# Kernel tuning notes

Hardware: AMD Instinct MI355X
Metric: run time of the kernel (lower is better)

Reference implementation:

```python
import jax, jax.numpy as jnp
import numpy as np

B, N, C, H = 4, 2048, 1024, 16
D = C // H

def setup_inputs() -> dict:
    key = jax.random.key(0)
    k1, k2, k3 = jax.random.split(key, 3)
    x = jax.random.normal(k1, (B, N, C), dtype=jnp.float32)
    w_qkv = jax.random.normal(k2, (C, 3 * C), dtype=jnp.float32) * (C ** -0.5)
    w_proj = jax.random.normal(k3, (C, C), dtype=jnp.float32) * (C ** -0.5)
    b_proj = jnp.zeros((C,), dtype=jnp.float32)
    return {"x": x, "w_qkv": w_qkv, "w_proj": w_proj, "b_proj": b_proj}

def reference(x, w_qkv, w_proj, b_proj):
    scale = D ** -0.5
    qkv = x @ w_qkv                                   # [B,N,3C]
    qkv = qkv.reshape(B, N, 3, H, D).transpose(2, 0, 3, 1, 4)  # [3,B,H,N,D]
    q, k, v = qkv[0], qkv[1], qkv[2]
    attn = jnp.einsum('bhnd,bhmd->bhnm', q, k) * scale  # [B,H,N,N]
    attn = jax.nn.softmax(attn, axis=-1)
    o = jnp.einsum('bhnm,bhmd->bhnd', attn, v)          # [B,H,N,D]
    o = o.transpose(0, 2, 1, 3).reshape(B, N, C)
    return o @ w_proj + b_proj
```

## Files before the change

### kernel.cpp

```cpp
#include <hip/hip_runtime.h>
#include <hip/hip_bf16.h>


#define B_ 4
#define N_ 2048
#define C_ 1024
#define H_ 16
#define D_ 64
#define KVB 128
#define MCONST 24.0f

typedef __attribute__((ext_vector_type(8))) __bf16 bf16x8;
typedef __attribute__((ext_vector_type(4))) float f32x4;
typedef unsigned int u32;

__device__ inline unsigned short f2bf(float f) {
  __bf16 h = (__bf16)f;
  return __builtin_bit_cast(unsigned short, h);
}

__device__ __forceinline__ void gld16(const void* g, void* l) {
  __builtin_amdgcn_global_load_lds(
      (const __attribute__((address_space(1))) u32*)g,
      (__attribute__((address_space(3))) u32*)l, 16, 0, 0);
}

__global__ __launch_bounds__(256) void cvt_bf16_kernel(
    const float* __restrict__ in, unsigned short* __restrict__ out) {
  int i = (blockIdx.x * 256 + threadIdx.x) * 8;
  float4 f0 = *(const float4*)&in[i];
  float4 f1 = *(const float4*)&in[i + 4];
  ushort4 h0, h1;
  h0.x = f2bf(f0.x); h0.y = f2bf(f0.y); h0.z = f2bf(f0.z); h0.w = f2bf(f0.w);
  h1.x = f2bf(f1.x); h1.y = f2bf(f1.y); h1.z = f2bf(f1.z); h1.w = f2bf(f1.w);
  *(ushort4*)&out[i] = h0;
  *(ushort4*)&out[i + 4] = h1;
}

__global__ __launch_bounds__(256) void transpose_cvt_kernel(
    const float* __restrict__ in, unsigned short* __restrict__ out,
    int K, int Nn) {
  __shared__ float tile[32][33];
  const int t = threadIdx.x;
  const int k0 = blockIdx.y * 32, n0 = blockIdx.x * 32;
  {
    int r = t >> 3, c = (t & 7) * 4;
    float4 f = *(const float4*)&in[(size_t)(k0 + r) * Nn + n0 + c];
    tile[r][c + 0] = f.x; tile[r][c + 1] = f.y;
    tile[r][c + 2] = f.z; tile[r][c + 3] = f.w;
  }
  __syncthreads();
  {
    int nr = t >> 3, kc = (t & 7) * 4;
    ushort4 h;
    h.x = f2bf(tile[kc + 0][nr]);
    h.y = f2bf(tile[kc + 1][nr]);
    h.z = f2bf(tile[kc + 2][nr]);
    h.w = f2bf(tile[kc + 3][nr]);
    *(ushort4*)&out[(size_t)(n0 + nr) * K + k0 + kc] = h;
  }
}

__global__ __launch_bounds__(256) void transpose_v_kernel(
    const unsigned short* __restrict__ vb, unsigned short* __restrict__ vtb) {
  __shared__ u32 tile[64][65];
  const int tid = threadIdx.x;
  const int n0 = blockIdx.x * 64;
  const int bh = blockIdx.y;
  const size_t base = (size_t)bh * N_ * D_;
#pragma unroll
  for (int i = 0; i < 2; i++) {
    int id = i * 256 + tid;
    int row = id >> 3, c8 = id & 7;
    uint4 v = *(const uint4*)&vb[base + (size_t)(n0 + row) * D_ + c8 * 8];
    const unsigned short* pv = (const unsigned short*)&v;
#pragma unroll
    for (int j = 0; j < 8; j++) tile[row][c8 * 8 + j] = pv[j];
  }
  __syncthreads();
#pragma unroll
  for (int i = 0; i < 2; i++) {
    int id = i * 256 + tid;
    int d = id >> 3, nc = id & 7;
    uint4 o;
    unsigned short* po = (unsigned short*)&o;
#pragma unroll
    for (int j = 0; j < 8; j++) po[j] = (unsigned short)tile[nc * 8 + j][d];
    *(uint4*)&vtb[base + (size_t)d * N_ + n0 + nc * 8] = o;
  }
}

template<int MODE>
__global__ __launch_bounds__(256) void gemm128_kernel(
    const unsigned short* __restrict__ A, const unsigned short* __restrict__ Bt,
    const float* __restrict__ bias,
    unsigned short* __restrict__ qb, unsigned short* __restrict__ kb,
    unsigned short* __restrict__ vb, float* __restrict__ outp,
    int M, int K, int Nout)
{
  __shared__ unsigned short Al[128 * 64];
  __shared__ unsigned short Bl[128 * 64];
  const int tid = threadIdx.x;
  const int w = tid >> 6, lane = tid & 63;
  const int l15 = lane & 15, lk = lane >> 4;
  const int wr = w >> 1, wc = w & 1;
  const int n0 = blockIdx.x * 128, m0 = blockIdx.y * 128;
  const int srow = tid >> 3;
  const int scol = (tid & 7) * 8;

  f32x4 acc[4][4];
#pragma unroll
  for (int m = 0; m < 4; m++)
#pragma unroll
    for (int n = 0; n < 4; n++) acc[m][n] = f32x4{0.f, 0.f, 0.f, 0.f};

  for (int kt = 0; kt < K; kt += 64) {
#pragma unroll
    for (int i = 0; i < 4; i++)
      gld16(&A[(size_t)(m0 + i * 32 + srow) * K + kt + scol],
            &Al[i * 2048 + w * 512]);
#pragma unroll
    for (int i = 0; i < 4; i++)
      gld16(&Bt[(size_t)(n0 + i * 32 + srow) * K + kt + scol],
            &Bl[i * 2048 + w * 512]);
    __syncthreads();

#pragma unroll
    for (int kk = 0; kk < 2; kk++) {
      bf16x8 af[4], bf[4];
#pragma unroll
      for (int m = 0; m < 4; m++)
        af[m] = *(const bf16x8*)&Al[(wr * 64 + m * 16 + l15) * 64 + kk * 32 + lk * 8];
#pragma unroll
      for (int n = 0; n < 4; n++)
        bf[n] = *(const bf16x8*)&Bl[(wc * 64 + n * 16 + l15) * 64 + kk * 32 + lk * 8];
#pragma unroll
      for (int m = 0; m < 4; m++)
#pragma unroll
        for (int n = 0; n < 4; n++)
          acc[m][n] = __builtin_amdgcn_mfma_f32_16x16x32_bf16(af[m], bf[n], acc[m][n], 0, 0, 0);
    }
    __syncthreads();
  }

  if (MODE == 0) {
#pragma unroll
    for (int n = 0; n < 4; n++) {
      int c = n0 + wc * 64 + n * 16 + l15;
      int tsel = c >> 10, h = (c >> 6) & 15, d = c & 63;
      unsigned short* dst = (tsel == 0) ? qb : (tsel == 1 ? kb : vb);
      float sc = (tsel == 0) ? 0.125f * 1.44269504088896340736f : 1.0f;
#pragma unroll
      for (int m = 0; m < 4; m++) {
#pragma unroll
        for (int r = 0; r < 4; r++) {
          int row = m0 + wr * 64 + m * 16 + lk * 4 + r;
          int b = row >> 11, nn = row & 2047;
          dst[(((size_t)(b * 16 + h)) * 2048 + nn) * 64 + d] = f2bf(acc[m][n][r] * sc);
        }
      }
    }
  } else {
#pragma unroll
    for (int n = 0; n < 4; n++) {
      int c = n0 + wc * 64 + n * 16 + l15;
      float bv = bias[c];
#pragma unroll
      for (int m = 0; m < 4; m++) {
#pragma unroll
        for (int r = 0; r < 4; r++) {
          int row = m0 + wr * 64 + m * 16 + lk * 4 + r;
          outp[(size_t)row * Nout + c] = acc[m][n][r] + bv;
        }
      }
    }
  }
}

__global__ __launch_bounds__(256) void flash_kernel(
    const unsigned short* __restrict__ qb, const unsigned short* __restrict__ kb,
    const unsigned short* __restrict__ vtb, unsigned short* __restrict__ ob)
{
  __shared__ unsigned short Kl[KVB * 64];
  __shared__ unsigned short Vl[64 * KVB];
  __shared__ unsigned short Pl[64][136];
  const int tid = threadIdx.x;
  const int w = tid >> 6;
  const int lane = tid & 63;
  const int l15 = lane & 15, lk = lane >> 4;
  const int q0 = blockIdx.x * 64;
  const int bh = blockIdx.y;
  const size_t base = (size_t)bh * N_ * D_;
  const unsigned short* Qg = qb + base;
  const unsigned short* Kg = kb + base;
  const unsigned short* Vtg = vtb + base;

  const int k_r  = tid >> 3;
  const int k_sl = (tid & 7) ^ (k_r & 7);
  const int v_r  = tid >> 4;
  const int v_sl = ((tid & 15) & 8) | ((tid & 7) ^ (v_r & 7));

  bf16x8 qf[2];
#pragma unroll
  for (int kk = 0; kk < 2; kk++)
    qf[kk] = *(const bf16x8*)&Qg[(size_t)(q0 + w * 16 + l15) * 64 + kk * 32 + lk * 8];

  f32x4 acc_o[4];
#pragma unroll
  for (int i = 0; i < 4; i++) acc_o[i] = f32x4{0.f, 0.f, 0.f, 0.f};
  float lrow[4];
#pragma unroll
  for (int r = 0; r < 4; r++) lrow[r] = 0.f;

  const int swz = (l15 & 7) << 3;
  const int prswz = (l15 & 8) << 1;

  for (int kv0 = 0; kv0 < N_; kv0 += KVB) {
#pragma unroll
    for (int i = 0; i < 4; i++)
      gld16(&Kg[(size_t)(kv0 + i * 32 + k_r) * 64 + k_sl * 8],
            &Kl[i * 2048 + w * 512]);
#pragma unroll
    for (int i = 0; i < 4; i++)
      gld16(&Vtg[(size_t)(i * 16 + v_r) * N_ + kv0 + v_sl * 8],
            &Vl[i * 2048 + w * 512]);
    __syncthreads();

    f32x4 sa[8];
#pragma unroll
    for (int i = 0; i < 8; i++)
      sa[i] = f32x4{-MCONST, -MCONST, -MCONST, -MCONST};
    __builtin_amdgcn_s_setprio(1);
#pragma unroll
    for (int kk = 0; kk < 2; kk++) {
#pragma unroll
      for (int nf = 0; nf < 8; nf++) {
        bf16x8 b = *(const bf16x8*)&Kl[(nf * 16 + l15) * 64 + ((kk * 32 + lk * 8) ^ swz)];
        sa[nf] = __builtin_amdgcn_mfma_f32_16x16x32_bf16(qf[kk], b, sa[nf], 0, 0, 0);
      }
    }
    __builtin_amdgcn_s_setprio(0);

#pragma unroll
    for (int r = 0; r < 4; r++) {
      float p0 = __builtin_amdgcn_exp2f(sa[0][r]);
      float p1 = __builtin_amdgcn_exp2f(sa[1][r]);
      float p2 = __builtin_amdgcn_exp2f(sa[2][r]);
      float p3 = __builtin_amdgcn_exp2f(sa[3][r]);
      float p4 = __builtin_amdgcn_exp2f(sa[4][r]);
      float p5 = __builtin_amdgcn_exp2f(sa[5][r]);
      float p6 = __builtin_amdgcn_exp2f(sa[6][r]);
      float p7 = __builtin_amdgcn_exp2f(sa[7][r]);
      lrow[r] += ((p0 + p1) + (p2 + p3)) + ((p4 + p5) + (p6 + p7));
      int prow = w * 16 + lk * 4 + r;
      int pswz = (prow & 8) << 1;
      Pl[prow][(0   + l15) ^ pswz] = f2bf(p0);
      Pl[prow][(16  + l15) ^ pswz] = f2bf(p1);
      Pl[prow][(32  + l15) ^ pswz] = f2bf(p2);
      Pl[prow][(48  + l15) ^ pswz] = f2bf(p3);
      Pl[prow][(64  + l15) ^ pswz] = f2bf(p4);
      Pl[prow][(80  + l15) ^ pswz] = f2bf(p5);
      Pl[prow][(96  + l15) ^ pswz] = f2bf(p6);
      Pl[prow][(112 + l15) ^ pswz] = f2bf(p7);
    }

    __builtin_amdgcn_s_setprio(1);
#pragma unroll
    for (int kk = 0; kk < 4; kk++) {
      bf16x8 a = *(const bf16x8*)&Pl[w * 16 + l15][(kk * 32 + lk * 8) ^ prswz];
#pragma unroll
      for (int nf = 0; nf < 4; nf++) {
        bf16x8 b = *(const bf16x8*)&Vl[(nf * 16 + l15) * 128 + ((kk * 32 + lk * 8) ^ swz)];
        acc_o[nf] = __builtin_amdgcn_mfma_f32_16x16x32_bf16(a, b, acc_o[nf], 0, 0, 0);
      }
    }
    __builtin_amdgcn_s_setprio(0);
    __syncthreads();
  }

#pragma unroll
  for (int r = 0; r < 4; r++) {
    float rs = lrow[r];
    rs += __shfl_xor(rs, 1);
    rs += __shfl_xor(rs, 2);
    rs += __shfl_xor(rs, 4);
    rs += __shfl_xor(rs, 8);
    lrow[r] = rs;
  }

  const int b = bh >> 4, h = bh & 15;
#pragma unroll
  for (int r = 0; r < 4; r++) {
    float inv = 1.0f / lrow[r];
    int n = q0 + w * 16 + lk * 4 + r;
    size_t obase = (((size_t)b * N_ + n) * H_ + h) * D_;
#pragma unroll
    for (int nf = 0; nf < 4; nf++)
      ob[obase + nf * 16 + l15] = f2bf(acc_o[nf][r] * inv);
  }
}

extern "C" void kernel_launch(void* const* d_in, const int* in_sizes, int n_in,
                              void* d_out, int out_size, void* d_ws, size_t ws_size,
                              hipStream_t stream) {
  const float* x      = (const float*)d_in[0];
  const float* w_qkv  = (const float*)d_in[1];
  const float* w_proj = (const float*)d_in[2];
  const float* b_proj = (const float*)d_in[3];
  float* out = (float*)d_out;

  const size_t qsz = (size_t)B_ * H_ * N_ * D_;
  unsigned short* qb     = (unsigned short*)d_ws;
  unsigned short* kb     = qb + qsz;
  unsigned short* vb     = kb + qsz;
  unsigned short* vtb    = vb + qsz;
  unsigned short* xbf    = vtb + qsz;
  unsigned short* ob     = xbf;
  unsigned short* wqkv_t = xbf + qsz;
  unsigned short* wproj_t= wqkv_t + (size_t)3072 * 1024;

  cvt_bf16_kernel<<<4096, 256, 0, stream>>>(x, xbf);
  transpose_cvt_kernel<<<dim3(3072 / 32, 1024 / 32), 256, 0, stream>>>(w_qkv, wqkv_t, 1024, 3072);
  transpose_cvt_kernel<<<dim3(1024 / 32, 1024 / 32), 256, 0, stream>>>(w_proj, wproj_t, 1024, 1024);

  gemm128_kernel<0><<<dim3(3072 / 128, 8192 / 128), 256, 0, stream>>>(
      xbf, wqkv_t, nullptr, qb, kb, vb, nullptr, 8192, 1024, 3072);

  transpose_v_kernel<<<dim3(N_ / 64, B_ * H_), 256, 0, stream>>>(vb, vtb);

  flash_kernel<<<dim3(N_ / 64, B_ * H_), 256, 0, stream>>>(qb, kb, vtb, ob);

  gemm128_kernel<1><<<dim3(1024 / 128, 8192 / 128), 256, 0, stream>>>(
      ob, wproj_t, b_proj, nullptr, nullptr, nullptr, out, 8192, 1024, 1024);
}
```

Baseline: 251.2 us.

## Use 32x32 MFMA with register-resident P in flash attention

Rewrites the flash-attention inner loop around 32x32x16 bf16 MFMAs. S is computed as K·Q^T, so the exponentiated probabilities can be packed to bf16 and rearranged with a cross-half lane shuffle straight into the A operand of the PV MFMA. This removes the shared-memory P round trip and its LDS traffic. Each block now handles 128 query rows (32 per wave) with 64-key tiles, which doubles K/V reuse per load but halves the grid and adds shuffle and select work plus a final LDS exchange of row sums.

```diff
diff --git a/kernel.cpp b/kernel.cpp
--- a/kernel.cpp
+++ b/kernel.cpp
@@ -7,16 +7,21 @@
 #define C_ 1024
 #define H_ 16
 #define D_ 64
-#define KVB 128
 #define MCONST 24.0f
 
 typedef __attribute__((ext_vector_type(8))) __bf16 bf16x8;
 typedef __attribute__((ext_vector_type(4))) float f32x4;
+typedef __attribute__((ext_vector_type(16))) float f32x16;
 typedef unsigned int u32;
+typedef __attribute__((ext_vector_type(4))) u32 u32x4;
 
 __device__ inline unsigned short f2bf(float f) {
   __bf16 h = (__bf16)f;
   return __builtin_bit_cast(unsigned short, h);
+}
+
+__device__ __forceinline__ u32 pk2(float lo, float hi) {
+  return (u32)f2bf(lo) | ((u32)f2bf(hi) << 16);
 }
 
 __device__ __forceinline__ void gld16(const void* g, void* l) {
@@ -181,122 +186,107 @@
     const unsigned short* __restrict__ qb, const unsigned short* __restrict__ kb,
     const unsigned short* __restrict__ vtb, unsigned short* __restrict__ ob)
 {
-  __shared__ unsigned short Kl[KVB * 64];
-  __shared__ unsigned short Vl[64 * KVB];
-  __shared__ unsigned short Pl[64][136];
+  __shared__ unsigned short Kl[64 * 64];
+  __shared__ unsigned short Vl[64 * 64];
+  __shared__ float Lf[128];
   const int tid = threadIdx.x;
   const int w = tid >> 6;
   const int lane = tid & 63;
-  const int l15 = lane & 15, lk = lane >> 4;
-  const int q0 = blockIdx.x * 64;
+  const int l31 = lane & 31;
+  const int hi = lane >> 5;
+  const int q0 = blockIdx.x * 128;
   const int bh = blockIdx.y;
   const size_t base = (size_t)bh * N_ * D_;
   const unsigned short* Qg = qb + base;
   const unsigned short* Kg = kb + base;
   const unsigned short* Vtg = vtb + base;
 
-  const int k_r  = tid >> 3;
-  const int k_sl = (tid & 7) ^ (k_r & 7);
-  const int v_r  = tid >> 4;
-  const int v_sl = ((tid & 15) & 8) | ((tid & 7) ^ (v_r & 7));
-
-  bf16x8 qf[2];
-#pragma unroll
-  for (int kk = 0; kk < 2; kk++)
-    qf[kk] = *(const bf16x8*)&Qg[(size_t)(q0 + w * 16 + l15) * 64 + kk * 32 + lk * 8];
-
-  f32x4 acc_o[4];
-#pragma unroll
-  for (int i = 0; i < 4; i++) acc_o[i] = f32x4{0.f, 0.f, 0.f, 0.f};
-  float lrow[4];
-#pragma unroll
-  for (int r = 0; r < 4; r++) lrow[r] = 0.f;
-
-  const int swz = (l15 & 7) << 3;
-  const int prswz = (l15 & 8) << 1;
-
-  for (int kv0 = 0; kv0 < N_; kv0 += KVB) {
-#pragma unroll
-    for (int i = 0; i < 4; i++)
-      gld16(&Kg[(size_t)(kv0 + i * 32 + k_r) * 64 + k_sl * 8],
+  const int s_r = tid >> 3;
+  const int s_sl = (tid & 7) ^ (s_r & 7);
+  const int swz = (lane & 7) << 3;
+
+  const int qrow_g = q0 + w * 32 + l31;
+  bf16x8 qf[4];
+#pragma unroll
+  for (int ds = 0; ds < 4; ds++)
+    qf[ds] = *(const bf16x8*)&Qg[(size_t)qrow_g * 64 + ds * 16 + hi * 8];
+
+  f32x16 acc0, acc1, minit;
+#pragma unroll
+  for (int i = 0; i < 16; i++) { acc0[i] = 0.f; acc1[i] = 0.f; minit[i] = -MCONST; }
+  float lrow = 0.f;
+
+  for (int kv0 = 0; kv0 < N_; kv0 += 64) {
+#pragma unroll
+    for (int i = 0; i < 2; i++)
+      gld16(&Kg[(size_t)(kv0 + i * 32 + s_r) * 64 + s_sl * 8],
             &Kl[i * 2048 + w * 512]);
 #pragma unroll
-    for (int i = 0; i < 4; i++)
-      gld16(&Vtg[(size_t)(i * 16 + v_r) * N_ + kv0 + v_sl * 8],
+    for (int i = 0; i < 2; i++)
+      gld16(&Vtg[(size_t)(i * 32 + s_r) * N_ + kv0 + s_sl * 8],
             &Vl[i * 2048 + w * 512]);
     __syncthreads();
 
-    f32x4 sa[8];
-#pragma unroll
-    for (int i = 0; i < 8; i++)
-      sa[i] = f32x4{-MCONST, -MCONST, -MCONST, -MCONST};
+    u32 F[4][4];
+#pragma unroll
+    for (int t = 0; t < 2; t++) {
+      f32x16 sa = minit;
+      __builtin_amdgcn_s_setprio(1);
+#pragma unroll
+      for (int ds = 0; ds < 4; ds++) {
+        bf16x8 a = *(const bf16x8*)&Kl[(t * 32 + l31) * 64 + ((ds * 16 + hi * 8) ^ swz)];
+        sa = __builtin_amdgcn_mfma_f32_32x32x16_bf16(a, qf[ds], sa, 0, 0, 0);
+      }
+      __builtin_amdgcn_s_setprio(0);
+
+      float p[16];
+#pragma unroll
+      for (int r = 0; r < 16; r++) p[r] = __builtin_amdgcn_exp2f(sa[r]);
+      lrow += ((p[0] + p[1]) + (p[2] + p[3])) + ((p[4] + p[5]) + (p[6] + p[7]))
+            + ((p[8] + p[9]) + (p[10] + p[11])) + ((p[12] + p[13]) + (p[14] + p[15]));
+
+      u32 pk[8], sw[8];
+#pragma unroll
+      for (int j = 0; j < 8; j++) pk[j] = pk2(p[2 * j], p[2 * j + 1]);
+#pragma unroll
+      for (int j = 0; j < 8; j++) sw[j] = (u32)__shfl_xor((int)pk[j], 32);
+      F[2 * t][0] = hi ? sw[2] : pk[0];
+      F[2 * t][1] = hi ? sw[3] : pk[1];
+      F[2 * t][2] = hi ? pk[2] : sw[0];
+      F[2 * t][3] = hi ? pk[3] : sw[1];
+      F[2 * t + 1][0] = hi ? sw[6] : pk[4];
+      F[2 * t + 1][1] = hi ? sw[7] : pk[5];
+      F[2 * t + 1][2] = hi ? pk[6] : sw[4];
+      F[2 * t + 1][3] = hi ? pk[7] : sw[5];
+    }
+
     __builtin_amdgcn_s_setprio(1);
 #pragma unroll
-    for (int kk = 0; kk < 2; kk++) {
-#pragma unroll
-      for (int nf = 0; nf < 8; nf++) {
-        bf16x8 b = *(const bf16x8*)&Kl[(nf * 16 + l15) * 64 + ((kk * 32 + lk * 8) ^ swz)];
-        sa[nf] = __builtin_amdgcn_mfma_f32_16x16x32_bf16(qf[kk], b, sa[nf], 0, 0, 0);
-      }
-    }
-    __builtin_amdgcn_s_setprio(0);
-
-#pragma unroll
-    for (int r = 0; r < 4; r++) {
-      float p0 = __builtin_amdgcn_exp2f(sa[0][r]);
-      float p1 = __builtin_amdgcn_exp2f(sa[1][r]);
-      float p2 = __builtin_amdgcn_exp2f(sa[2][r]);
-      float p3 = __builtin_amdgcn_exp2f(sa[3][r]);
-      float p4 = __builtin_amdgcn_exp2f(sa[4][r]);
-      float p5 = __builtin_amdgcn_exp2f(sa[5][r]);
-      float p6 = __builtin_amdgcn_exp2f(sa[6][r]);
-      float p7 = __builtin_amdgcn_exp2f(sa[7][r]);
-      lrow[r] += ((p0 + p1) + (p2 + p3)) + ((p4 + p5) + (p6 + p7));
-      int prow = w * 16 + lk * 4 + r;
-      int pswz = (prow & 8) << 1;
-      Pl[prow][(0   + l15) ^ pswz] = f2bf(p0);
-      Pl[prow][(16  + l15) ^ pswz] = f2bf(p1);
-      Pl[prow][(32  + l15) ^ pswz] = f2bf(p2);
-      Pl[prow][(48  + l15) ^ pswz] = f2bf(p3);
-      Pl[prow][(64  + l15) ^ pswz] = f2bf(p4);
-      Pl[prow][(80  + l15) ^ pswz] = f2bf(p5);
-      Pl[prow][(96  + l15) ^ pswz] = f2bf(p6);
-      Pl[prow][(112 + l15) ^ pswz] = f2bf(p7);
-    }
-
-    __builtin_amdgcn_s_setprio(1);
-#pragma unroll
-    for (int kk = 0; kk < 4; kk++) {
-      bf16x8 a = *(const bf16x8*)&Pl[w * 16 + l15][(kk * 32 + lk * 8) ^ prswz];
-#pragma unroll
-      for (int nf = 0; nf < 4; nf++) {
-        bf16x8 b = *(const bf16x8*)&Vl[(nf * 16 + l15) * 128 + ((kk * 32 + lk * 8) ^ swz)];
-        acc_o[nf] = __builtin_amdgcn_mfma_f32_16x16x32_bf16(a, b, acc_o[nf], 0, 0, 0);
-      }
+    for (int ks = 0; ks < 4; ks++) {
+      u32x4 fv = {F[ks][0], F[ks][1], F[ks][2], F[ks][3]};
+      bf16x8 a = __builtin_bit_cast(bf16x8, fv);
+      bf16x8 b0 = *(const bf16x8*)&Vl[(0 * 32 + l31) * 64 + ((ks * 16 + hi * 8) ^ swz)];
+      acc0 = __builtin_amdgcn_mfma_f32_32x32x16_bf16(a, b0, acc0, 0, 0, 0);
+      bf16x8 b1 = *(const bf16x8*)&Vl[(1 * 32 + l31) * 64 + ((ks * 16 + hi * 8) ^ swz)];
+      acc1 = __builtin_amdgcn_mfma_f32_32x32x16_bf16(a, b1, acc1, 0, 0, 0);
     }
     __builtin_amdgcn_s_setprio(0);
     __syncthreads();
   }
 
-#pragma unroll
-  for (int r = 0; r < 4; r++) {
-    float rs = lrow[r];
-    rs += __shfl_xor(rs, 1);
-    rs += __shfl_xor(rs, 2);
-    rs += __shfl_xor(rs, 4);
-    rs += __shfl_xor(rs, 8);
-    lrow[r] = rs;
-  }
+  float rs = lrow + __shfl_xor(lrow, 32);
+  if (lane < 32) Lf[w * 32 + l31] = rs;
+  __syncthreads();
 
   const int b = bh >> 4, h = bh & 15;
 #pragma unroll
-  for (int r = 0; r < 4; r++) {
-    float inv = 1.0f / lrow[r];
-    int n = q0 + w * 16 + lk * 4 + r;
-    size_t obase = (((size_t)b * N_ + n) * H_ + h) * D_;
-#pragma unroll
-    for (int nf = 0; nf < 4; nf++)
-      ob[obase + nf * 16 + l15] = f2bf(acc_o[nf][r] * inv);
+  for (int r = 0; r < 16; r++) {
+    int qr = (r & 3) + 8 * (r >> 2) + 4 * hi;
+    float inv = 1.0f / Lf[w * 32 + qr];
+    int nq = q0 + w * 32 + qr;
+    size_t ob0 = (((size_t)b * N_ + nq) * H_ + h) * D_;
+    ob[ob0 + l31]      = f2bf(acc0[r] * inv);
+    ob[ob0 + 32 + l31] = f2bf(acc1[r] * inv);
   }
 }
 
@@ -328,7 +318,7 @@
 
   transpose_v_kernel<<<dim3(N_ / 64, B_ * H_), 256, 0, stream>>>(vb, vtb);
 
-  flash_kernel<<<dim3(N_ / 64, B_ * H_), 256, 0, stream>>>(qb, kb, vtb, ob);
+  flash_kernel<<<dim3(N_ / 128, B_ * H_), 256, 0, stream>>>(qb, kb, vtb, ob);
 
   gemm128_kernel<1><<<dim3(1024 / 128, 8192 / 128), 256, 0, stream>>>(
       ob, wproj_t, b_proj, nullptr, nullptr, nullptr, out, 8192, 1024, 1024);
```

Result: faster. 244.8 us (-2.6%).
